# Kernel tuning notes

Measured on AMD Instinct MI355X. Metric: run time of the kernel, lower is better.

## Reference

```python
import jax, jax.numpy as jnp
import numpy as np

BN_EPS = 1e-5
CURVE_LENGTH = 8

def _gumbel_st(logits):
    # straight-through gumbel-softmax (no gumbel noise, temperature=1), over last dim
    y = jax.nn.softmax(logits, axis=-1)
    ind = jnp.argmax(y, axis=-1)
    y_hard = jax.nn.one_hot(ind, logits.shape[-1], dtype=y.dtype)
    return jax.lax.stop_gradient(y_hard - y) + y

def _crossover(cur_vec, nb):
    # cur_vec: (B, c), nb: (B, c, k) -> clamp(1 + cosine, 0, 1), detached
    cur_vec = jax.lax.stop_gradient(cur_vec)
    nb = jax.lax.stop_gradient(nb)
    dot = jnp.einsum('bc,bck->bk', cur_vec, nb)
    n1 = jnp.linalg.norm(cur_vec, axis=1, keepdims=True)        # (B, 1)
    n2 = jnp.linalg.norm(nb, axis=1)                            # (B, k)
    cos = dot / jnp.maximum(n1 * n2, 1e-8)
    return jnp.clip(1.0 + cos, 0.0, 1.0)

def walk_forward(x, adj, cur, agent_w, agent_gamma, agent_beta, agent_mean, agent_var,
                 mom_w, mom_gamma, mom_beta, mom_mean, mom_var):
    bn, c, tot = x.shape
    k = adj.shape[-1]
    cn = cur.shape[1]
    flatten_x = jnp.transpose(x, (0, 2, 1)).reshape(bn * tot, c)
    offset = (jnp.arange(bn, dtype=adj.dtype) * tot)[:, None, None]
    tmp_adj = (adj + offset).reshape(bn * tot, k)
    flatten_cur = (cur + offset).reshape(-1)                    # (bn*cn,)
    inv_agent = agent_gamma / jnp.sqrt(agent_var + BN_EPS)      # (1,)
    inv_mom = mom_gamma / jnp.sqrt(mom_var + BN_EPS)            # (2,)
    rows = jnp.arange(bn * cn)
    curves = []
    pre_feature = cur_feature = cur_feature_cos = pre_feature_cos = None
    for step in range(CURVE_LENGTH):
        if step == 0:
            pre_feature = jnp.transpose(flatten_x[flatten_cur].reshape(bn, cn, c, 1), (0, 2, 1, 3))  # (bn,c,cn,1)
        else:
            cat1 = jnp.concatenate([cur_feature[..., 0], pre_feature[..., 0]], axis=1)  # (bn,2c,cn)
            mlog = jnp.einsum('bcn,oc->bon', cat1, mom_w)
            mlog = (mlog - mom_mean[None, :, None]) * inv_mom[None, :, None] + mom_beta[None, :, None]
            att = jax.nn.softmax(mlog, axis=1).reshape(bn, 1, cn, 2)  # faithful to torch .view
            cat2 = jnp.concatenate([cur_feature, pre_feature], axis=-1)  # (bn,c,cn,2)
            pre_feature = jnp.sum(cat2 * att, axis=-1, keepdims=True)    # (bn,c,cn,1)
            pre_feature_cos = jnp.transpose(pre_feature, (0, 2, 1, 3)).reshape(bn * cn, c)
        pick_idx = tmp_adj[flatten_cur]                                  # (bn*cn, k)
        pv_flat = flatten_x[pick_idx.reshape(-1)].reshape(bn * cn, k, c)
        pv_cos = jnp.transpose(pv_flat, (0, 2, 1))                       # (bn*cn, c, k)
        pick_values = jnp.transpose(pv_flat.reshape(bn, cn, k, c), (0, 3, 1, 2))  # (bn,c,cn,k)
        cat3 = jnp.concatenate([pick_values, jnp.broadcast_to(pre_feature, pick_values.shape)], axis=1)  # (bn,2c,cn,k)
        logits = jnp.einsum('bcnk,c->bnk', cat3, agent_w)[:, None]       # conv2d 1x1 -> (bn,1,cn,k)
        logits = (logits - agent_mean[0]) * inv_agent[0] + agent_beta[0]
        if step != 0:
            d = _crossover(cur_feature_cos - pre_feature_cos, pv_cos - cur_feature_cos[..., None])
            logits = logits * d.reshape(bn, cn, k)[:, None]
        sel = _gumbel_st(logits)                                         # (bn,1,cn,k)
        cur_feature = jnp.sum(pick_values * sel, axis=-1, keepdims=True)  # (bn,c,cn,1)
        cur_feature_cos = jnp.transpose(cur_feature, (0, 2, 1, 3)).reshape(bn * cn, c)
        cur_idx = jnp.argmax(sel, axis=-1).reshape(-1)                   # (bn*cn,)
        flatten_cur = pick_idx[rows, cur_idx]
        curves.append(cur_feature)
    return jnp.concatenate(curves, axis=-1)  # (bn, c, cn, curve_length)

def setup_inputs() -> dict:
    key = jax.random.key(0)
    ks = jax.random.split(key, 12)
    bn, c, tot, k, cn = 16, 64, 8192, 20, 512
    xyz = jax.random.normal(ks[0], (bn, 3, tot), dtype=jnp.float32)
    x = jax.random.normal(ks[1], (bn, c, tot), dtype=jnp.float32)
    adj = jax.random.randint(ks[2], (bn, tot, k), 0, tot)
    cur = jax.random.randint(ks[3], (bn, cn, 1), 0, tot)
    sc = 1.0 / np.sqrt(2 * c)
    agent_w = jax.random.normal(ks[4], (2 * c,), dtype=jnp.float32) * sc
    mom_w = jax.random.normal(ks[5], (2, 2 * c), dtype=jnp.float32) * sc
    agent_gamma = 1.0 + 0.1 * jax.random.normal(ks[6], (1,), dtype=jnp.float32)
    agent_beta = 0.1 * jax.random.normal(ks[7], (1,), dtype=jnp.float32)
    agent_mean = 0.1 * jax.random.normal(ks[8], (1,), dtype=jnp.float32)
    agent_var = jax.random.uniform(ks[9], (1,), minval=0.5, maxval=1.5, dtype=jnp.float32)
    mom_gamma = 1.0 + 0.1 * jax.random.normal(ks[10], (2,), dtype=jnp.float32)
    mom_beta = 0.1 * jax.random.normal(ks[11], (2,), dtype=jnp.float32)
    mom_mean = 0.1 * jax.random.normal(jax.random.fold_in(key, 101), (2,), dtype=jnp.float32)
    mom_var = jax.random.uniform(jax.random.fold_in(key, 102), (2,), minval=0.5, maxval=1.5, dtype=jnp.float32)
    return {"xyz": xyz, "x": x, "adj": adj, "cur": cur,
            "agent_w": agent_w, "agent_gamma": agent_gamma, "agent_beta": agent_beta,
            "agent_mean": agent_mean, "agent_var": agent_var,
            "mom_w": mom_w, "mom_gamma": mom_gamma, "mom_beta": mom_beta,
            "mom_mean": mom_mean, "mom_var": mom_var}

def reference(xyz, x, adj, cur, agent_w, agent_gamma, agent_beta, agent_mean, agent_var,
              mom_w, mom_gamma, mom_beta, mom_mean, mom_var):
    # xyz is accepted (as in the torch forward) but never used: the original code
    # calls `xyz.transpose(1, 2).contiguous` without invoking it.
    return walk_forward(x, adj, cur, agent_w, agent_gamma, agent_beta, agent_mean,
                        agent_var, mom_w, mom_gamma, mom_beta, mom_mean, mom_var)
```

## Files before the change

kernel.cpp:

```cpp
#include <hip/hip_runtime.h>
#include <cmath>

#define BN 16
#define CDIM 64
#define TOT 8192
#define KNB 20
#define CN 512
#define NSTEPS 8
#define WPB 16
#define BPB 32
#define WSTRIDE 577
#define FLAGSTRIDE 32
#define MAGIC 0x5A17ECE1u

typedef float vf4 __attribute__((ext_vector_type(4)));

__device__ __forceinline__ float dot4(float a, float b, float c, float d,
                                      float wa, float wb, float wc, float wd) {
  return a * wa + b * wb + c * wc + d * wd;
}

template <int CTRL>
__device__ __forceinline__ float dpp_add(float v) {
  int o = __builtin_amdgcn_update_dpp(0, __float_as_int(v), CTRL, 0xF, 0xF, true);
  return v + __int_as_float(o);
}

__device__ __forceinline__ float gred16(float v) {
  v = dpp_add<0xB1>(v);
  v = dpp_add<0x4E>(v);
  v = dpp_add<0x141>(v);
  v = dpp_add<0x140>(v);
  return v;
}

__global__ __launch_bounds__(256, 2) void walk_kernel(
    const float* __restrict__ x, const int* __restrict__ adj, const int* __restrict__ cur,
    const float* __restrict__ agent_w, const float* __restrict__ agent_gamma,
    const float* __restrict__ agent_beta, const float* __restrict__ agent_mean,
    const float* __restrict__ agent_var, const float* __restrict__ mom_w,
    const float* __restrict__ mom_gamma, const float* __restrict__ mom_beta,
    const float* __restrict__ mom_mean, const float* __restrict__ mom_var,
    float* __restrict__ xt, float* __restrict__ pa,
    float* __restrict__ out, float* __restrict__ sbuf, unsigned int* __restrict__ flags) {
  __shared__ float lds_out[WPB * WSTRIDE];
  const int tid  = threadIdx.x;
  const int lane = tid & 63;
  const int wv   = tid >> 6;
  const int g    = lane >> 4;
  const int L    = lane & 15;
  const int b     = (blockIdx.x & 7) + (((blockIdx.x >> 8) & 1) << 3);
  const int chunk = (blockIdx.x >> 3) & 31;
  const int w     = wv * 4 + g;
  const int n     = chunk * WPB + w;
  const int c0    = L << 2;
  const int P0    = (chunk & 15) << 1;

  unsigned int* myflag = flags + ((size_t)b * BPB + chunk) * FLAGSTRIDE;

  {
    float (*tile)[65] = (float (*)[65])lds_out;
#pragma unroll 1
    for (int i = 0; i < 4; ++i) {
      const int t0 = ((chunk << 2) + i) << 6;
#pragma unroll
      for (int k = 0; k < 4; ++k) {
        int fid = tid + k * 256;
        int cc = fid >> 4, qt = (fid & 15) << 2;
        float4 vv = *(const float4*)(x + ((size_t)b * CDIM + cc) * TOT + t0 + qt);
        tile[cc][qt + 0] = vv.x; tile[cc][qt + 1] = vv.y;
        tile[cc][qt + 2] = vv.z; tile[cc][qt + 3] = vv.w;
      }
      __syncthreads();
#pragma unroll
      for (int k = 0; k < 4; ++k) {
        int fid = tid + k * 256;
        int tt = fid >> 4, qc = (fid & 15) << 2;
        vf4 vv = {tile[qc + 0][tt], tile[qc + 1][tt], tile[qc + 2][tt], tile[qc + 3][tt]};
        float* dst = xt + ((size_t)b * TOT + t0 + tt) * CDIM + qc;
        asm volatile("global_store_dwordx4 %0, %1, off sc0 sc1" :: "v"(dst), "v"(vv) : "memory");
      }
      if (tid < 64) {
        const int tt = tid;
        float q[16];
#pragma unroll
        for (int l = 0; l < 16; ++l)
          q[l] = dot4(tile[4 * l][tt], tile[4 * l + 1][tt],
                      tile[4 * l + 2][tt], tile[4 * l + 3][tt],
                      agent_w[4 * l], agent_w[4 * l + 1],
                      agent_w[4 * l + 2], agent_w[4 * l + 3]);
        float sA = (q[0] + q[1]) + (q[2] + q[3]);
        float sB = (q[4] + q[5]) + (q[6] + q[7]);
        float sC = (q[8] + q[9]) + (q[10] + q[11]);
        float sD = (q[12] + q[13]) + (q[14] + q[15]);
        __hip_atomic_store(pa + (size_t)b * TOT + t0 + tt, (sA + sB) + (sC + sD),
                           __ATOMIC_RELAXED, __HIP_MEMORY_SCOPE_AGENT);
      }
      __syncthreads();
    }
    asm volatile("s_waitcnt vmcnt(0)" ::: "memory");
    __builtin_amdgcn_s_barrier();
    if (tid == 0)
      __hip_atomic_store(myflag + 8, MAGIC, __ATOMIC_RELAXED, __HIP_MEMORY_SCOPE_AGENT);
    if (tid < BPB) {
      const unsigned int* f = flags + ((size_t)b * BPB + tid) * FLAGSTRIDE + 8;
      while (__hip_atomic_load(f, __ATOMIC_RELAXED, __HIP_MEMORY_SCOPE_AGENT) != MAGIC)
        __builtin_amdgcn_s_sleep(2);
    }
    __builtin_amdgcn_s_barrier();
    asm volatile("" ::: "memory");
  }

  const vf4 aw2  = *(const vf4*)(agent_w + 64 + c0);
  const vf4 mw0a = *(const vf4*)(mom_w + c0);
  const vf4 mw0b = *(const vf4*)(mom_w + 64 + c0);
  const vf4 mw1a = *(const vf4*)(mom_w + 128 + c0);
  const vf4 mw1b = *(const vf4*)(mom_w + 192 + c0);
  const float amean  = agent_mean[0];
  const float abeta  = agent_beta[0];
  const float ainv   = agent_gamma[0] / sqrtf(agent_var[0] + 1e-5f);
  const float m0mean = mom_mean[0], m1mean = mom_mean[1];
  const float m0inv  = mom_gamma[0] / sqrtf(mom_var[0] + 1e-5f);
  const float m1inv  = mom_gamma[1] / sqrtf(mom_var[1] + 1e-5f);
  const float m0beta = mom_beta[0], m1beta = mom_beta[1];

  const float* xb   = xt + (size_t)b * TOT * CDIM;
  const float* pab  = pa + (size_t)b * TOT;
  const int*   adjb = adj + (size_t)b * TOT * KNB;
  float*       lout = lds_out + w * WSTRIDE;

  int t = cur[b * CN + n];
  vf4 pf = *(const vf4*)(xb + (size_t)t * CDIM + c0);
  vf4 cf = pf;
  vf4 u  = (vf4){0.f, 0.f, 0.f, 0.f};

  int   idx[KNB];
  vf4   nv[KNB];
  float pav[KNB];
  {
    const int4* arow = (const int4*)(adjb + (size_t)t * KNB);
    int4 q0 = arow[0], q1 = arow[1], q2 = arow[2], q3 = arow[3], q4 = arow[4];
    int tmp[KNB] = {q0.x, q0.y, q0.z, q0.w, q1.x, q1.y, q1.z, q1.w,
                    q2.x, q2.y, q2.z, q2.w, q3.x, q3.y, q3.z, q3.w,
                    q4.x, q4.y, q4.z, q4.w};
#pragma unroll
    for (int j = 0; j < KNB; ++j) idx[j] = tmp[j];
#pragma unroll
    for (int j = 0; j < KNB; ++j) {
      nv[j]  = *(const vf4*)(xb + (size_t)idx[j] * CDIM + c0);
      pav[j] = pab[idx[j]];
    }
  }

#pragma unroll 1
  for (int s = 0; s < NSTEPS; ++s) {
    float n1 = 0.f;
    if (s > 0) {
      const float* sb = sbuf + ((size_t)(b * NSTEPS + s) << 10);
      float A0 = __hip_atomic_load(sb + 2 * n, __ATOMIC_RELAXED, __HIP_MEMORY_SCOPE_AGENT);
      float A1 = __hip_atomic_load(sb + 2 * n + 1, __ATOMIC_RELAXED, __HIP_MEMORY_SCOPE_AGENT);
      pf.x = A0 * cf.x + A1 * pf.x;
      pf.y = A0 * cf.y + A1 * pf.y;
      pf.z = A0 * cf.z + A1 * pf.z;
      pf.w = A0 * cf.w + A1 * pf.w;
      u.x = cf.x - pf.x; u.y = cf.y - pf.y; u.z = cf.z - pf.z; u.w = cf.w - pf.w;
      n1 = sqrtf(gred16(u.x * u.x + u.y * u.y + u.z * u.z + u.w * u.w));
    }
    float pw = gred16(pf.x * aw2.x + pf.y * aw2.y + pf.z * aw2.z + pf.w * aw2.w);

    float bestp = -3.4e38f;
    int   bestt = 0;
    vf4   bestv = (vf4){0.f, 0.f, 0.f, 0.f};
#pragma unroll
    for (int j = 0; j < KNB; ++j) {
      const vf4 v = nv[j];
      float logit = (pav[j] + pw - amean) * ainv + abeta;
      float p;
      if (s > 0) {
        float tx = v.x - cf.x, ty = v.y - cf.y, tz = v.z - cf.z, tw = v.w - cf.w;
        float su = tx * u.x + ty * u.y + tz * u.z + tw * u.w;
        float sn = tx * tx + ty * ty + tz * tz + tw * tw;
        su = gred16(su);
        sn = gred16(sn);
        float den  = fmaxf(n1 * sqrtf(sn), 1e-8f);
        float cosv = su * __builtin_amdgcn_rcpf(den);
        float dfac = fminf(fmaxf(1.0f + cosv, 0.0f), 1.0f);
        p = logit * dfac;
      } else {
        p = logit;
      }
      if (p > bestp) { bestp = p; bestt = idx[j]; bestv = v; }
    }
    cf = bestv;
    t  = bestt;
    lout[(c0 + 0) * 9 + s] = cf.x;
    lout[(c0 + 1) * 9 + s] = cf.y;
    lout[(c0 + 2) * 9 + s] = cf.z;
    lout[(c0 + 3) * 9 + s] = cf.w;

    if (s < NSTEPS - 1) {
      float p0 = cf.x * mw0a.x + cf.y * mw0a.y + cf.z * mw0a.z + cf.w * mw0a.w +
                 pf.x * mw0b.x + pf.y * mw0b.y + pf.z * mw0b.z + pf.w * mw0b.w;
      float p1 = cf.x * mw1a.x + cf.y * mw1a.y + cf.z * mw1a.z + cf.w * mw1a.w +
                 pf.x * mw1b.x + pf.y * mw1b.y + pf.z * mw1b.z + pf.w * mw1b.w;
      p0 = gred16(p0);
      p1 = gred16(p1);
      float mlog0 = (p0 - m0mean) * m0inv + m0beta;
      float mlog1 = (p1 - m1mean) * m1inv + m1beta;
      float mx = fmaxf(mlog0, mlog1);
      float e0 = expf(mlog0 - mx), e1 = expf(mlog1 - mx);
      float sinv = 1.0f / (e0 + e1);
      float* sb = sbuf + ((size_t)(b * NSTEPS + s + 1) << 10);
      if (L == 0) {
        __hip_atomic_store(sb + n, e0 * sinv, __ATOMIC_RELAXED, __HIP_MEMORY_SCOPE_AGENT);
        __hip_atomic_store(sb + CN + n, e1 * sinv, __ATOMIC_RELAXED, __HIP_MEMORY_SCOPE_AGENT);
      }
      asm volatile("s_waitcnt vmcnt(0)" ::: "memory");
      __builtin_amdgcn_s_barrier();
      if (tid == 0)
        __hip_atomic_store(myflag + (s + 1), MAGIC, __ATOMIC_RELAXED, __HIP_MEMORY_SCOPE_AGENT);
      const int4* arow = (const int4*)(adjb + (size_t)t * KNB);
      int4 q0 = arow[0], q1 = arow[1], q2 = arow[2], q3 = arow[3], q4 = arow[4];
      int tmp[KNB] = {q0.x, q0.y, q0.z, q0.w, q1.x, q1.y, q1.z, q1.w,
                      q2.x, q2.y, q2.z, q2.w, q3.x, q3.y, q3.z, q3.w,
                      q4.x, q4.y, q4.z, q4.w};
#pragma unroll
      for (int j = 0; j < KNB; ++j) idx[j] = tmp[j];
#pragma unroll
      for (int j = 0; j < KNB; ++j) {
        nv[j]  = *(const vf4*)(xb + (size_t)idx[j] * CDIM + c0);
        pav[j] = pab[idx[j]];
      }
      if (lane == 0 && wv < 2) {
        const unsigned int* pflag =
            flags + ((size_t)b * BPB + P0 + wv) * FLAGSTRIDE + (s + 1);
        while (__hip_atomic_load(pflag, __ATOMIC_RELAXED, __HIP_MEMORY_SCOPE_AGENT) != MAGIC)
          __builtin_amdgcn_s_sleep(2);
      }
      __builtin_amdgcn_s_barrier();
      asm volatile("" ::: "memory");
    }
  }

#pragma unroll
  for (int e = 0; e < 4; ++e) {
    const float* src = lout + (c0 + e) * 9;
    float4 w0 = make_float4(src[0], src[1], src[2], src[3]);
    float4 w1 = make_float4(src[4], src[5], src[6], src[7]);
    float* op = out + (((size_t)(b * CDIM + c0 + e) * CN) + n) * NSTEPS;
    *(float4*)(op)     = w0;
    *(float4*)(op + 4) = w1;
  }
}

extern "C" void kernel_launch(void* const* d_in, const int* in_sizes, int n_in,
                              void* d_out, int out_size, void* d_ws, size_t ws_size,
                              hipStream_t stream) {
  (void)in_sizes; (void)n_in; (void)out_size; (void)ws_size;
  const float* x          = (const float*)d_in[1];
  const int*   adj        = (const int*)d_in[2];
  const int*   cur        = (const int*)d_in[3];
  const float* agent_w    = (const float*)d_in[4];
  const float* agent_gamma= (const float*)d_in[5];
  const float* agent_beta = (const float*)d_in[6];
  const float* agent_mean = (const float*)d_in[7];
  const float* agent_var  = (const float*)d_in[8];
  const float* mom_w      = (const float*)d_in[9];
  const float* mom_gamma  = (const float*)d_in[10];
  const float* mom_beta   = (const float*)d_in[11];
  const float* mom_mean   = (const float*)d_in[12];
  const float* mom_var    = (const float*)d_in[13];
  float* out = (float*)d_out;

  char* ws = (char*)d_ws;
  const size_t xt_bytes   = (size_t)BN * TOT * CDIM * sizeof(float);
  const size_t sbuf_bytes = (size_t)BN * NSTEPS * 2 * CN * sizeof(float);
  const size_t pa_bytes   = (size_t)BN * TOT * sizeof(float);
  float*        xt    = (float*)ws;
  float*        sbuf  = (float*)(ws + xt_bytes);
  float*        pab   = (float*)(ws + xt_bytes + sbuf_bytes);
  unsigned int* flags = (unsigned int*)(ws + xt_bytes + sbuf_bytes + pa_bytes);

  walk_kernel<<<BN * BPB, 256, 0, stream>>>(x, adj, cur, agent_w, agent_gamma, agent_beta,
                                            agent_mean, agent_var, mom_w, mom_gamma, mom_beta,
                                            mom_mean, mom_var, xt, pab, out, sbuf, flags);
}
```

Baseline: 163.1 us.

## Replace per-block step barriers with per-wave flags and targeted peer waits

Each wave now publishes its own step counter flag and spins only on the two producer waves whose attention weights it needs, instead of a block-wide barrier plus block flag and a wait on two producer blocks. The point is to cut block-level sync overhead and let waves move ahead independently between walk steps. The attention loads move ahead of the neighbour gathers, which puts the spin wait on the critical path before the prefetch. Every lane of each wave now spins on global flags, and the flags only ever increase, so correctness across repeated launches depends on the workspace being reset between runs.

```diff
diff --git a/kernel.cpp b/kernel.cpp
--- a/kernel.cpp
+++ b/kernel.cpp
@@ -9,8 +9,9 @@
 #define NSTEPS 8
 #define WPB 16
 #define BPB 32
+#define WVB 128
 #define WSTRIDE 577
-#define FLAGSTRIDE 32
+#define LINE 32
 #define MAGIC 0x5A17ECE1u
 
 typedef float vf4 __attribute__((ext_vector_type(4)));
@@ -42,7 +43,8 @@
     const float* __restrict__ mom_gamma, const float* __restrict__ mom_beta,
     const float* __restrict__ mom_mean, const float* __restrict__ mom_var,
     float* __restrict__ xt, float* __restrict__ pa,
-    float* __restrict__ out, float* __restrict__ sbuf, unsigned int* __restrict__ flags) {
+    float* __restrict__ out, float* __restrict__ sbuf,
+    unsigned int* __restrict__ pflag, int* __restrict__ wflag) {
   __shared__ float lds_out[WPB * WSTRIDE];
   const int tid  = threadIdx.x;
   const int lane = tid & 63;
@@ -54,9 +56,9 @@
   const int w     = wv * 4 + g;
   const int n     = chunk * WPB + w;
   const int c0    = L << 2;
-  const int P0    = (chunk & 15) << 1;
-
-  unsigned int* myflag = flags + ((size_t)b * BPB + chunk) * FLAGSTRIDE;
+  const int W     = (chunk << 2) + wv;
+  const int P0    = (W << 1) & (WVB - 1);
+  const int P1    = ((W << 1) + 1) & (WVB - 1);
 
   {
     float (*tile)[65] = (float (*)[65])lds_out;
@@ -101,9 +103,10 @@
     asm volatile("s_waitcnt vmcnt(0)" ::: "memory");
     __builtin_amdgcn_s_barrier();
     if (tid == 0)
-      __hip_atomic_store(myflag + 8, MAGIC, __ATOMIC_RELAXED, __HIP_MEMORY_SCOPE_AGENT);
+      __hip_atomic_store(pflag + ((size_t)b * BPB + chunk) * LINE, MAGIC,
+                         __ATOMIC_RELAXED, __HIP_MEMORY_SCOPE_AGENT);
     if (tid < BPB) {
-      const unsigned int* f = flags + ((size_t)b * BPB + tid) * FLAGSTRIDE + 8;
+      const unsigned int* f = pflag + ((size_t)b * BPB + tid) * LINE;
       while (__hip_atomic_load(f, __ATOMIC_RELAXED, __HIP_MEMORY_SCOPE_AGENT) != MAGIC)
         __builtin_amdgcn_s_sleep(2);
     }
@@ -128,11 +131,13 @@
   const float* pab  = pa + (size_t)b * TOT;
   const int*   adjb = adj + (size_t)b * TOT * KNB;
   float*       lout = lds_out + w * WSTRIDE;
+  int*         wfb  = wflag + (size_t)b * WVB * LINE;
 
   int t = cur[b * CN + n];
   vf4 pf = *(const vf4*)(xb + (size_t)t * CDIM + c0);
   vf4 cf = pf;
   vf4 u  = (vf4){0.f, 0.f, 0.f, 0.f};
+  float A0v = 0.f, A1v = 0.f;
 
   int   idx[KNB];
   vf4   nv[KNB];
@@ -156,13 +161,10 @@
   for (int s = 0; s < NSTEPS; ++s) {
     float n1 = 0.f;
     if (s > 0) {
-      const float* sb = sbuf + ((size_t)(b * NSTEPS + s) << 10);
-      float A0 = __hip_atomic_load(sb + 2 * n, __ATOMIC_RELAXED, __HIP_MEMORY_SCOPE_AGENT);
-      float A1 = __hip_atomic_load(sb + 2 * n + 1, __ATOMIC_RELAXED, __HIP_MEMORY_SCOPE_AGENT);
-      pf.x = A0 * cf.x + A1 * pf.x;
-      pf.y = A0 * cf.y + A1 * pf.y;
-      pf.z = A0 * cf.z + A1 * pf.z;
-      pf.w = A0 * cf.w + A1 * pf.w;
+      pf.x = A0v * cf.x + A1v * pf.x;
+      pf.y = A0v * cf.y + A1v * pf.y;
+      pf.z = A0v * cf.z + A1v * pf.z;
+      pf.w = A0v * cf.w + A1v * pf.w;
       u.x = cf.x - pf.x; u.y = cf.y - pf.y; u.z = cf.z - pf.z; u.w = cf.w - pf.w;
       n1 = sqrtf(gred16(u.x * u.x + u.y * u.y + u.z * u.z + u.w * u.w));
     }
@@ -216,9 +218,19 @@
         __hip_atomic_store(sb + CN + n, e1 * sinv, __ATOMIC_RELAXED, __HIP_MEMORY_SCOPE_AGENT);
       }
       asm volatile("s_waitcnt vmcnt(0)" ::: "memory");
-      __builtin_amdgcn_s_barrier();
-      if (tid == 0)
-        __hip_atomic_store(myflag + (s + 1), MAGIC, __ATOMIC_RELAXED, __HIP_MEMORY_SCOPE_AGENT);
+      if (lane == 0)
+        __hip_atomic_store(wfb + W * LINE, s + 1, __ATOMIC_RELAXED, __HIP_MEMORY_SCOPE_AGENT);
+      {
+        const int* f0 = wfb + P0 * LINE;
+        const int* f1 = wfb + P1 * LINE;
+        while (__hip_atomic_load(f0, __ATOMIC_RELAXED, __HIP_MEMORY_SCOPE_AGENT) <= s ||
+               __hip_atomic_load(f1, __ATOMIC_RELAXED, __HIP_MEMORY_SCOPE_AGENT) <= s)
+          __builtin_amdgcn_s_sleep(1);
+      }
+      asm volatile("" ::: "memory");
+      const float* sbr = sbuf + ((size_t)(b * NSTEPS + s + 1) << 10);
+      A0v = __hip_atomic_load(sbr + 2 * n, __ATOMIC_RELAXED, __HIP_MEMORY_SCOPE_AGENT);
+      A1v = __hip_atomic_load(sbr + 2 * n + 1, __ATOMIC_RELAXED, __HIP_MEMORY_SCOPE_AGENT);
       const int4* arow = (const int4*)(adjb + (size_t)t * KNB);
       int4 q0 = arow[0], q1 = arow[1], q2 = arow[2], q3 = arow[3], q4 = arow[4];
       int tmp[KNB] = {q0.x, q0.y, q0.z, q0.w, q1.x, q1.y, q1.z, q1.w,
@@ -231,14 +243,6 @@
         nv[j]  = *(const vf4*)(xb + (size_t)idx[j] * CDIM + c0);
         pav[j] = pab[idx[j]];
       }
-      if (lane == 0 && wv < 2) {
-        const unsigned int* pflag =
-            flags + ((size_t)b * BPB + P0 + wv) * FLAGSTRIDE + (s + 1);
-        while (__hip_atomic_load(pflag, __ATOMIC_RELAXED, __HIP_MEMORY_SCOPE_AGENT) != MAGIC)
-          __builtin_amdgcn_s_sleep(2);
-      }
-      __builtin_amdgcn_s_barrier();
-      asm volatile("" ::: "memory");
     }
   }
 
@@ -276,12 +280,14 @@
   const size_t xt_bytes   = (size_t)BN * TOT * CDIM * sizeof(float);
   const size_t sbuf_bytes = (size_t)BN * NSTEPS * 2 * CN * sizeof(float);
   const size_t pa_bytes   = (size_t)BN * TOT * sizeof(float);
+  const size_t pf_bytes   = (size_t)BN * BPB * LINE * sizeof(unsigned);
   float*        xt    = (float*)ws;
   float*        sbuf  = (float*)(ws + xt_bytes);
   float*        pab   = (float*)(ws + xt_bytes + sbuf_bytes);
-  unsigned int* flags = (unsigned int*)(ws + xt_bytes + sbuf_bytes + pa_bytes);
+  unsigned int* pflag = (unsigned int*)(ws + xt_bytes + sbuf_bytes + pa_bytes);
+  int*          wflag = (int*)(ws + xt_bytes + sbuf_bytes + pa_bytes + pf_bytes);
 
   walk_kernel<<<BN * BPB, 256, 0, stream>>>(x, adj, cur, agent_w, agent_gamma, agent_beta,
                                             agent_mean, agent_var, mom_w, mom_gamma, mom_beta,
-                                            mom_mean, mom_var, xt, pab, out, sbuf, flags);
-}
+                                            mom_mean, mom_var, xt, pab, out, sbuf, pflag, wflag);
+}
```

New measurement: 166.9 us. 1.02x slower.
